# Kernel tuning notes

Hardware: AMD Instinct MI355X
Metric: run time of the kernel (lower is better)

The kernel has to match this reference:

```python
import jax, jax.numpy as jnp
import numpy as np

N = 207      # nodes (hardcoded in source)
D = 128      # hid_dim
H = 8        # attention heads
C = D // H   # head dim
L = 4        # num_layers
B = 16       # batch
NO = 3       # number of orbits
SZ = 69      # orbit size
EPS = 1e-5
SLOPE = 0.2  # GATv2 leaky_relu negative slope


def _cat_matrix():
    # edge category for pair (i,j): off-diag -> pos_i*NO+pos_j, diag -> NO^2+pos_i
    pos = np.arange(N) // SZ
    c = pos[:, None] * NO + pos[None, :]
    np.fill_diagonal(c, NO * NO + pos)
    return c  # [N, N] int


def setup_inputs() -> dict:
    key = jax.random.key(0)
    ks = jax.random.split(key, 16)
    s = 0.05
    rn = lambda k, shape: jax.random.normal(k, shape, jnp.float32) * s
    return {
        "x": jax.random.normal(ks[0], (B, N, 6), jnp.float32),
        "cat": jnp.asarray(_cat_matrix(), jnp.int32),          # [N,N] edge categories
        "emb": rn(ks[1], (NO * NO + NO, D)),                   # edge embedding table
        "in1_W": rn(ks[2], (D, 6)), "in1_b": jnp.zeros((D,)),
        "ln1_g": jnp.ones((D,)), "ln1_b": jnp.zeros((D,)),
        "in2_W": rn(ks[3], (D, D)), "in2_b": jnp.zeros((D,)),
        "ln2_g": jnp.ones((D,)), "ln2_b": jnp.zeros((D,)),
        "Wl": rn(ks[4], (L, D, D)), "bl": jnp.zeros((L, D)),   # GATv2 lin_l (source)
        "Wr": rn(ks[5], (L, D, D)), "br": jnp.zeros((L, D)),   # GATv2 lin_r (target)
        "We": rn(ks[6], (L, D, D)),                            # GATv2 lin_edge (no bias)
        "att": rn(ks[7], (L, H, C)),                           # attention vector
        "cb": jnp.zeros((L, D)),                               # conv output bias
        "pW": rn(ks[8], (L, D, D)), "pb": jnp.zeros((L, D)),   # projection layers
        "lng": jnp.ones((L, D)), "lnb": jnp.zeros((L, D)),     # per-layer LayerNorm
        "oW": rn(ks[9], (2, D)), "ob": jnp.zeros((2,)),        # output layer
    }


def _ln(x, g, b):
    m = x.mean(-1, keepdims=True)
    v = ((x - m) ** 2).mean(-1, keepdims=True)
    return (x - m) * jax.lax.rsqrt(v + EPS) * g + b


def _fwd(cat, x, emb, in1_W, in1_b, ln1_g, ln1_b, in2_W, in2_b, ln2_g, ln2_b,
         Wl, bl, Wr, br, We, att, cb, pW, pb, lng, lnb, oW, ob):
    # input MLP: Linear -> LN -> ReLU -> Linear -> LN
    h = jax.nn.relu(_ln(x @ in1_W.T + in1_b, ln1_g, ln1_b))
    h = _ln(h @ in2_W.T + in2_b, ln2_g, ln2_b)                 # [B,N,D]
    e_all = emb[cat]                                           # [N,N,D] per-edge embedding
    for l in range(L):
        h_prev = h
        gs = (h @ Wl[l].T + bl[l]).reshape(B, N, H, C)         # source transform
        gd = (h @ Wr[l].T + br[l]).reshape(B, N, H, C)         # target transform
        ee = (e_all @ We[l].T).reshape(N, N, H, C)             # edge transform
        # per-edge GATv2 score: edge (i -> j), i source, j target
        z = jax.nn.leaky_relu(gs[:, :, None] + gd[:, None, :] + ee[None], SLOPE)  # [B,i,j,H,C]
        a = jnp.einsum('bijhc,hc->bijh', z, att[l])
        a = jax.nn.softmax(a, axis=1)                          # softmax over sources per target
        o = jnp.einsum('bijh,bihc->bjhc', a, gs).reshape(B, N, D) + cb[l]
        h = h_prev + jax.nn.relu(_ln(o @ pW[l].T + pb[l], lng[l], lnb[l]))
    return h @ oW.T + ob                                       # [B,N,2]


def reference(x, cat, emb, in1_W, in1_b, ln1_g, ln1_b, in2_W, in2_b, ln2_g, ln2_b,
              Wl, bl, Wr, br, We, att, cb, pW, pb, lng, lnb, oW, ob):
    return _fwd(cat, x, emb, in1_W, in1_b, ln1_g, ln1_b, in2_W, in2_b, ln2_g, ln2_b,
                Wl, bl, Wr, br, We, att, cb, pW, pb, lng, lnb, oW, ob)
```

## Files before the change

### kernel.cpp

```cpp
#include <hip/hip_runtime.h>
#include <hip/hip_bf16.h>

#define NN 207
#define DD 128
#define LL 4
#define BB 16
#define ROWS (BB*NN)
#define RB 8
#define LBLK (ROWS/RB)
#define EPSV 1e-5f
#define SLOPE 0.2f
#define GT4B (32*208*4)

template<bool BF>
__device__ __forceinline__ float ldin(const void* p, int i) {
    if (BF) {
        unsigned short u = ((const unsigned short*)p)[i];
        return __uint_as_float(((unsigned)u) << 16);
    } else {
        return ((const float*)p)[i];
    }
}

template<bool BF>
__device__ __forceinline__ void ldw32(const void* W, int base, float* w) {
    if (BF) {
        const uint4* p = (const uint4*)((const unsigned short*)W + base);
#pragma unroll
        for (int q = 0; q < 4; q++) {
            uint4 u = p[q];
            w[q*8+0] = __uint_as_float(u.x << 16);
            w[q*8+1] = __uint_as_float(u.x & 0xFFFF0000u);
            w[q*8+2] = __uint_as_float(u.y << 16);
            w[q*8+3] = __uint_as_float(u.y & 0xFFFF0000u);
            w[q*8+4] = __uint_as_float(u.z << 16);
            w[q*8+5] = __uint_as_float(u.z & 0xFFFF0000u);
            w[q*8+6] = __uint_as_float(u.w << 16);
            w[q*8+7] = __uint_as_float(u.w & 0xFFFF0000u);
        }
    } else {
        const float4* p = (const float4*)((const float*)W + base);
#pragma unroll
        for (int q = 0; q < 8; q++) {
            float4 u = p[q];
            w[q*4+0] = u.x; w[q*4+1] = u.y; w[q*4+2] = u.z; w[q*4+3] = u.w;
        }
    }
}

template<bool BF>
__device__ __forceinline__ float rowdot(const void* W, int rowbase, const float* sh) {
    float acc = 0.f;
    if (BF) {
        const uint4* p = (const uint4*)((const unsigned short*)W + rowbase);
#pragma unroll
        for (int q = 0; q < DD / 8; q++) {
            uint4 u = p[q];
            const float* s = sh + q * 8;
            acc += __uint_as_float(u.x << 16)        * s[0];
            acc += __uint_as_float(u.x & 0xFFFF0000u) * s[1];
            acc += __uint_as_float(u.y << 16)        * s[2];
            acc += __uint_as_float(u.y & 0xFFFF0000u) * s[3];
            acc += __uint_as_float(u.z << 16)        * s[4];
            acc += __uint_as_float(u.z & 0xFFFF0000u) * s[5];
            acc += __uint_as_float(u.w << 16)        * s[6];
            acc += __uint_as_float(u.w & 0xFFFF0000u) * s[7];
        }
    } else {
        const float4* p = (const float4*)((const float*)W + rowbase);
#pragma unroll
        for (int q = 0; q < DD / 4; q++) {
            float4 u = p[q];
            const float* s = sh + q * 4;
            acc += u.x * s[0]; acc += u.y * s[1]; acc += u.z * s[2]; acc += u.w * s[3];
        }
    }
    return acc;
}

__global__ void k_detect(const unsigned int* g1bits, int* flag) {
    *flag = (g1bits[0] == 0x3F803F80u) ? 1 : 0;
}

template<bool BF>
__device__ void et_body(float* sh, const void* emb, const void* We, float* et) {
    int l = blockIdx.x / 12, c = blockIdx.x % 12, d = threadIdx.x;
    sh[d] = ldin<BF>(emb, c * DD + d);
    __syncthreads();
    et[(l * 12 + c) * DD + d] = rowdot<BF>(We, l * DD * DD + d * DD, sh);
}
__global__ void k_et(const int* flag, const void* emb, const void* We, float* et) {
    __shared__ __align__(16) float smem[DD];
    if (*flag) et_body<true>(smem, emb, We, et);
    else       et_body<false>(smem, emb, We, et);
}

template<bool BF>
__device__ void mlp1_body(float* smem, const void* x, const void* W1, const void* b1,
                          const void* g1, const void* bv1, float* tmp) {
    float* s_x   = smem;
    float* so    = s_x + 48;
    float* stats = so + RB * 132;
    int r0 = blockIdx.x * RB, d = threadIdx.x;
    if (d < RB * 6) s_x[d] = ldin<BF>(x, r0 * 6 + d);
    __syncthreads();
    float w6[6];
#pragma unroll
    for (int k = 0; k < 6; k++) w6[k] = ldin<BF>(W1, d * 6 + k);
    float b0 = ldin<BF>(b1, d);
#pragma unroll
    for (int rr = 0; rr < RB; rr++) {
        float a = b0;
#pragma unroll
        for (int k = 0; k < 6; k++) a += w6[k] * s_x[rr * 6 + k];
        so[rr * 132 + d] = a;
    }
    __syncthreads();
    int rr2 = d >> 4, l16 = d & 15;
    float s = 0.f, sq = 0.f;
#pragma unroll
    for (int k = 0; k < 8; k++) { float v = so[rr2 * 132 + l16 + 16 * k]; s += v; sq += v * v; }
    s += __shfl_xor(s, 1); s += __shfl_xor(s, 2); s += __shfl_xor(s, 4); s += __shfl_xor(s, 8);
    sq += __shfl_xor(sq, 1); sq += __shfl_xor(sq, 2); sq += __shfl_xor(sq, 4); sq += __shfl_xor(sq, 8);
    if (l16 == 0) {
        float mean = s * (1.f / DD);
        float var = sq * (1.f / DD) - mean * mean;
        stats[rr2 * 2] = mean; stats[rr2 * 2 + 1] = rsqrtf(var + EPSV);
    }
    __syncthreads();
    float gv = ldin<BF>(g1, d), bb = ldin<BF>(bv1, d);
#pragma unroll
    for (int rr = 0; rr < RB; rr++) {
        float v = (so[rr * 132 + d] - stats[rr * 2]) * stats[rr * 2 + 1] * gv + bb;
        tmp[(r0 + rr) * DD + d] = fmaxf(v, 0.f);
    }
}
__global__ void k_mlp1(const int* flag, const void* x, const void* W1, const void* b1,
                       const void* g1, const void* bv1, float* tmp) {
    __shared__ __align__(16) float smem[48 + RB * 132 + RB * 2];
    if (*flag) mlp1_body<true>(smem, x, W1, b1, g1, bv1, tmp);
    else       mlp1_body<false>(smem, x, W1, b1, g1, bv1, tmp);
}

template<bool BF>
__device__ void lin_body(float* smem, int epi, const float* in, const void* W, int wOff,
                         const void* bias, const void* g, const void* bv, int dOff,
                         float* h) {
    float* sh    = smem;
    float* so    = sh + RB * DD;
    float* stats = so + RB * 132;
    int r0 = blockIdx.x * RB;
    int t = threadIdx.x, d = t & 127, half = t >> 7;
    float4* sh4 = (float4*)sh;
    const float4* iin = (const float4*)(in + r0 * DD);
    sh4[t] = iin[t];
    __syncthreads();
    float acc[4];
    float b0 = ldin<BF>(bias, dOff + d);
#pragma unroll
    for (int rr = 0; rr < 4; rr++) acc[rr] = b0;
#pragma unroll
    for (int c = 0; c < 4; c++) {
        float w[32];
        ldw32<BF>(W, wOff + d * DD + c * 32, w);
#pragma unroll
        for (int rr = 0; rr < 4; rr++) {
            const float* s = sh + (half * 4 + rr) * DD + c * 32;
            float a = acc[rr];
#pragma unroll
            for (int k = 0; k < 32; k++) a += s[k] * w[k];
            acc[rr] = a;
        }
    }
#pragma unroll
    for (int rr = 0; rr < 4; rr++) so[(half * 4 + rr) * 132 + d] = acc[rr];
    __syncthreads();
    int rr2 = t >> 5, l32 = t & 31;
    float s = 0.f, sq = 0.f;
#pragma unroll
    for (int k = 0; k < 4; k++) { float v = so[rr2 * 132 + l32 + 32 * k]; s += v; sq += v * v; }
    s += __shfl_xor(s, 1); s += __shfl_xor(s, 2); s += __shfl_xor(s, 4);
    s += __shfl_xor(s, 8); s += __shfl_xor(s, 16);
    sq += __shfl_xor(sq, 1); sq += __shfl_xor(sq, 2); sq += __shfl_xor(sq, 4);
    sq += __shfl_xor(sq, 8); sq += __shfl_xor(sq, 16);
    if (l32 == 0) {
        float mean = s * (1.f / DD);
        float var = sq * (1.f / DD) - mean * mean;
        stats[rr2 * 2] = mean; stats[rr2 * 2 + 1] = rsqrtf(var + EPSV);
    }
    __syncthreads();
    float gv = ldin<BF>(g, dOff + d), bb = ldin<BF>(bv, dOff + d);
#pragma unroll
    for (int rr = 0; rr < 4; rr++) {
        int row = half * 4 + rr;
        float v = (so[row * 132 + d] - stats[row * 2]) * stats[row * 2 + 1] * gv + bb;
        int rg = r0 + row;
        if (epi) h[(size_t)rg * DD + d] += fmaxf(v, 0.f);
        else     h[(size_t)rg * DD + d] = v;
    }
}
__global__ void k_lin(const int* flag, int epi, const float* in, const void* W, int wOff,
                      const void* bias, const void* g, const void* bv, int dOff, float* h) {
    __shared__ __align__(16) float smem[RB * DD + RB * 132 + RB * 2];
    if (*flag) lin_body<true>(smem, epi, in, W, wOff, bias, g, bv, dOff, h);
    else       lin_body<false>(smem, epi, in, W, wOff, bias, g, bv, dOff, h);
}

template<bool BF>
__device__ void gsgd_body(float* sh, int l, const float* h, const void* Wl, const void* bl,
                          const void* Wr, const void* br, float* gs, float* gd) {
    int r0 = blockIdx.x * RB;
    int t = threadIdx.x, d = t & 127, mat = t >> 7;
    float4* sh4 = (float4*)sh;
    const float4* hin = (const float4*)(h + r0 * DD);
    sh4[t] = hin[t];
    __syncthreads();
    const void* W  = mat ? Wr : Wl;
    const void* bv = mat ? br : bl;
    float acc[RB];
    float b0 = ldin<BF>(bv, l * DD + d);
#pragma unroll
    for (int rr = 0; rr < RB; rr++) acc[rr] = b0;
#pragma unroll
    for (int c = 0; c < 4; c++) {
        float w[32];
        ldw32<BF>(W, l * DD * DD + d * DD + c * 32, w);
#pragma unroll
        for (int rr = 0; rr < RB; rr++) {
            const float* s = sh + rr * DD + c * 32;
            float a = acc[rr];
#pragma unroll
            for (int k = 0; k < 32; k++) a += s[k] * w[k];
            acc[rr] = a;
        }
    }
    float* outp = mat ? gd : gs;
#pragma unroll
    for (int rr = 0; rr < RB; rr++) outp[(size_t)(r0 + rr) * DD + d] = acc[rr];
}
__global__ void k_gsgd(const int* flag, int l, const float* h, const void* Wl, const void* bl,
                       const void* Wr, const void* br, float* gs, float* gd) {
    __shared__ __align__(16) float smem[RB * DD];
    if (*flag) gsgd_body<true>(smem, l, h, Wl, bl, Wr, br, gs, gd);
    else       gsgd_body<false>(smem, l, h, Wl, bl, Wr, br, gs, gd);
}

__global__ void __launch_bounds__(256, 4) k_trans(const float* gs, float* gs_t4) {
    __shared__ __align__(16) float sb[RB * 132];
    int q = blockIdx.x;
    int batch = q / 26, pr = q - batch * 26;
    int brow0 = pr * 8;
    int nrows = NN - brow0; if (nrows > RB) nrows = RB;
    int t = threadIdx.x;
    int srow = t >> 5, se = t & 31;
    int cr = srow < nrows ? srow : nrows - 1;
    ((float4*)(sb + srow * 132))[se] =
        ((const float4*)(gs + (size_t)(batch * NN + brow0 + cr) * DD))[se];
    __syncthreads();
    int d4 = t >> 3, ii = t & 7;
    if (ii < nrows) {
        float4 v;
        v.x = sb[ii * 132 + d4 * 4 + 0];
        v.y = sb[ii * 132 + d4 * 4 + 1];
        v.z = sb[ii * 132 + d4 * 4 + 2];
        v.w = sb[ii * 132 + d4 * 4 + 3];
        ((float4*)(gs_t4 + (size_t)batch * GT4B))[d4 * 208 + brow0 + ii] = v;
    }
}

#define ATTN_SMEM (12*132 + 128 + 8*212 + 8 + 128 + 207)
template<bool BF>
__device__ void attn_body(float* smem, int l, const float* gs, const float* gd, const float* et,
                          const float* gs_t4, const int* cat, const void* att, const void* cb,
                          float* o) {
    float* s_ge   = smem;
    float* s_att  = s_ge + 12 * 132;
    float* s_pe   = s_att + 128;
    float* s_inv  = s_pe + 8 * 212;
    float* s_part = s_inv + 8;
    int*   s_cat  = (int*)(s_part + 128);
    int p = blockIdx.x;
    int r = (p & 7) * (ROWS / 8) + (p >> 3);
    int t = threadIdx.x, d = t & 127, seg = t >> 7;
    int b = r / NN, j = r - b * NN;
    if (t < DD) s_att[t] = ldin<BF>(att, l * DD + t);
    for (int idx = t; idx < NN; idx += 256) s_cat[idx] = cat[idx * NN + j];
    for (int idx = t; idx < 12 * DD; idx += 256) {
        int c = idx >> 7, k = idx & 127;
        s_ge[c * 132 + k] = et[l * 12 * DD + idx] + gd[(size_t)r * DD + k];
    }
    __syncthreads();
    const float* gsb = gs + (size_t)b * NN * DD;
    if (t < NN) {
        const float4* gt = ((const float4*)(gs_t4 + (size_t)b * GT4B)) + t;
        const float4* ge = (const float4*)(s_ge + s_cat[t] * 132);
        const float4* at = (const float4*)s_att;
        float acc[8];
#pragma unroll
        for (int hh = 0; hh < 8; hh++) acc[hh] = 0.f;
#pragma unroll
        for (int q = 0; q < 32; q++) {
            float4 g4 = gt[q * 208];
            float4 e4 = ge[q], a4 = at[q];
            float z0 = g4.x + e4.x, z1 = g4.y + e4.y, z2 = g4.z + e4.z, z3 = g4.w + e4.w;
            z0 = fmaxf(z0, SLOPE * z0); z1 = fmaxf(z1, SLOPE * z1);
            z2 = fmaxf(z2, SLOPE * z2); z3 = fmaxf(z3, SLOPE * z3);
            acc[q >> 2] += a4.x * z0 + a4.y * z1 + a4.z * z2 + a4.w * z3;
        }
#pragma unroll
        for (int hh = 0; hh < 8; hh++) s_pe[hh * 212 + t] = acc[hh];
    }
    __syncthreads();
    if (t < 128) {
        int hh = t >> 4, l16 = t & 15;
        float vals[13]; float mx = -1e30f;
#pragma unroll
        for (int k = 0; k < 13; k++) {
            int i = l16 + 16 * k;
            vals[k] = (i < NN) ? s_pe[hh * 212 + i] : -1e30f;
            mx = fmaxf(mx, vals[k]);
        }
        mx = fmaxf(mx, __shfl_xor(mx, 1)); mx = fmaxf(mx, __shfl_xor(mx, 2));
        mx = fmaxf(mx, __shfl_xor(mx, 4)); mx = fmaxf(mx, __shfl_xor(mx, 8));
        float sum = 0.f;
#pragma unroll
        for (int k = 0; k < 13; k++) {
            int i = l16 + 16 * k;
            float e = (i < NN) ? __expf(vals[k] - mx) : 0.f;
            if (i < 208) s_pe[hh * 212 + i] = e;
            sum += e;
        }
        sum += __shfl_xor(sum, 1); sum += __shfl_xor(sum, 2);
        sum += __shfl_xor(sum, 4); sum += __shfl_xor(sum, 8);
        if (l16 == 0) s_inv[hh] = 1.f / sum;
    }
    __syncthreads();
    {
        int hh = d >> 4;
        const float* ep = s_pe + hh * 212;
        const float* gp = gsb + d;
        float a0 = 0.f, a1 = 0.f, a2 = 0.f, a3 = 0.f;
        int i = seg * 104;
        int iend = seg ? NN : 104;
        for (; i + 8 <= iend; i += 8) {
            float g0 = gp[(i+0)*DD], g1 = gp[(i+1)*DD], g2 = gp[(i+2)*DD], g3 = gp[(i+3)*DD];
            float g4 = gp[(i+4)*DD], g5 = gp[(i+5)*DD], g6 = gp[(i+6)*DD], g7 = gp[(i+7)*DD];
            a0 = fmaf(ep[i+0], g0, a0); a1 = fmaf(ep[i+1], g1, a1);
            a2 = fmaf(ep[i+2], g2, a2); a3 = fmaf(ep[i+3], g3, a3);
            a0 = fmaf(ep[i+4], g4, a0); a1 = fmaf(ep[i+5], g5, a1);
            a2 = fmaf(ep[i+6], g6, a2); a3 = fmaf(ep[i+7], g7, a3);
        }
        for (; i < iend; i++) a0 = fmaf(ep[i], gp[i * DD], a0);
        float part = a0 + a1 + a2 + a3;
        if (seg) s_part[d] = part;
        __syncthreads();
        if (!seg) o[(size_t)r * DD + d] = (part + s_part[d]) * s_inv[hh] + ldin<BF>(cb, l * DD + d);
    }
}
__global__ void __launch_bounds__(256, 4)
k_attn(const int* flag, int l, const float* gs, const float* gd, const float* et,
       const float* gs_t4, const int* cat, const void* att, const void* cb,
       float* o) {
    __shared__ __align__(16) float smem[ATTN_SMEM];
    if (*flag) attn_body<true>(smem, l, gs, gd, et, gs_t4, cat, att, cb, o);
    else       attn_body<false>(smem, l, gs, gd, et, gs_t4, cat, att, cb, o);
}

__device__ __forceinline__ void blk_red2(float& a, float& b, float* red) {
#pragma unroll
    for (int m = 32; m; m >>= 1) { a += __shfl_xor(a, m); b += __shfl_xor(b, m); }
    int wid = threadIdx.x >> 6;
    if ((threadIdx.x & 63) == 0) { red[wid * 2] = a; red[wid * 2 + 1] = b; }
    __syncthreads();
    a = red[0] + red[2];
    b = red[1] + red[3];
    __syncthreads();
}
template<bool BF>
__device__ void out_body(float* red, const float* h, const void* oW, const void* ob, void* out) {
    int r = blockIdx.x, d = threadIdx.x;
    float hv = h[(size_t)r * DD + d];
    float p0 = hv * ldin<BF>(oW, d);
    float p1 = hv * ldin<BF>(oW, DD + d);
    blk_red2(p0, p1, red);
    if (d < 2) {
        float v = (d == 0 ? p0 : p1) + ldin<BF>(ob, d);
        if (BF) ((__hip_bfloat16*)out)[r * 2 + d] = __float2bfloat16(v);
        else    ((float*)out)[r * 2 + d] = v;
    }
}
__global__ void k_out(const int* flag, const float* h, const void* oW, const void* ob, void* out) {
    __shared__ float red[4];
    if (*flag) out_body<true>(red, h, oW, ob, out);
    else       out_body<false>(red, h, oW, ob, out);
}

extern "C" void kernel_launch(void* const* d_in, const int* in_sizes, int n_in,
                              void* d_out, int out_size, void* d_ws, size_t ws_size,
                              hipStream_t stream) {
    const void* x     = d_in[0];
    const int*  cat   = (const int*)d_in[1];
    const void* emb   = d_in[2];
    const void* in1W  = d_in[3];
    const void* in1b  = d_in[4];
    const void* ln1g  = d_in[5];
    const void* ln1b  = d_in[6];
    const void* in2W  = d_in[7];
    const void* in2b  = d_in[8];
    const void* ln2g  = d_in[9];
    const void* ln2b  = d_in[10];
    const void* Wl    = d_in[11];
    const void* bl    = d_in[12];
    const void* Wr    = d_in[13];
    const void* br    = d_in[14];
    const void* We    = d_in[15];
    const void* att   = d_in[16];
    const void* cb    = d_in[17];
    const void* pW    = d_in[18];
    const void* pb    = d_in[19];
    const void* lng   = d_in[20];
    const void* lnb   = d_in[21];
    const void* oW    = d_in[22];
    const void* ob    = d_in[23];

    float* ws  = (float*)d_ws;
    int*  flag = (int*)d_ws;
    float* h     = ws + 16;
    float* gs    = h    + ROWS * DD;
    float* gd    = gs   + ROWS * DD;
    float* o     = gd   + ROWS * DD;
    float* et    = o    + ROWS * DD;
    float* gs_t4 = et   + LL * 12 * DD;
    float* tmp   = gs;

    k_detect<<<1, 1, 0, stream>>>((const unsigned int*)ln1g, flag);
    k_et<<<LL * 12, DD, 0, stream>>>(flag, emb, We, et);
    k_mlp1<<<LBLK, DD, 0, stream>>>(flag, x, in1W, in1b, ln1g, ln1b, tmp);
    k_lin<<<LBLK, 256, 0, stream>>>(flag, 0, tmp, in2W, 0, in2b, ln2g, ln2b, 0, h);
    for (int l = 0; l < LL; l++) {
        k_gsgd<<<LBLK, 256, 0, stream>>>(flag, l, h, Wl, bl, Wr, br, gs, gd);
        k_trans<<<BB * 26, 256, 0, stream>>>(gs, gs_t4);
        k_attn<<<ROWS, 256, 0, stream>>>(flag, l, gs, gd, et, gs_t4, cat, att, cb, o);
        k_lin<<<LBLK, 256, 0, stream>>>(flag, 1, o, pW, l * DD * DD, pb, lng, lnb, l * DD, h);
    }
    k_out<<<ROWS, DD, 0, stream>>>(flag, h, oW, ob, d_out);
}
```

Baseline: 368.5 us.

## Process two target nodes per attention block to reuse source features

Each attention block now handles two target nodes (j and j+104) of the same batch, so the transposed source features loaded for scoring and the gs rows read in the aggregation step are shared across both targets. The grid shrinks from ROWS blocks to BB*104 blocks. The aggregation is reorganised so all 256 threads do float4 loads over 8 source segments, followed by a shared-memory reduction. In exchange it uses more shared memory and registers per block and has fewer blocks, which may lower occupancy.

```diff
diff --git a/kernel.cpp b/kernel.cpp
--- a/kernel.cpp
+++ b/kernel.cpp
@@ -268,93 +268,131 @@
     }
 }
 
-#define ATTN_SMEM (12*132 + 128 + 8*212 + 8 + 128 + 207)
+#define ATTN_SMEM (1584*2 + 128 + 1696*2 + 16 + 1024 + 416)
 template<bool BF>
 __device__ void attn_body(float* smem, int l, const float* gs, const float* gd, const float* et,
                           const float* gs_t4, const int* cat, const void* att, const void* cb,
                           float* o) {
-    float* s_ge   = smem;
-    float* s_att  = s_ge + 12 * 132;
-    float* s_pe   = s_att + 128;
-    float* s_inv  = s_pe + 8 * 212;
-    float* s_part = s_inv + 8;
-    int*   s_cat  = (int*)(s_part + 128);
+    float* s_ge1 = smem;
+    float* s_ge2 = s_ge1 + 1584;
+    float* s_att = s_ge2 + 1584;
+    float* s_pe1 = s_att + 128;
+    float* s_pe2 = s_pe1 + 1696;
+    float* s_inv = s_pe2 + 1696;
+    float* s_prt = s_inv + 16;
+    int*   s_cat1 = (int*)(s_prt + 1024);
+    int*   s_cat2 = s_cat1 + 208;
     int p = blockIdx.x;
-    int r = (p & 7) * (ROWS / 8) + (p >> 3);
-    int t = threadIdx.x, d = t & 127, seg = t >> 7;
-    int b = r / NN, j = r - b * NN;
+    int kk = (p & 7) * 208 + (p >> 3);
+    int b = kk / 104, k = kk - b * 104;
+    int j1 = k, j2 = k + 104;
+    bool has2 = (k < 103);
+    int r1 = b * NN + j1, r2 = b * NN + j2;
+    int t = threadIdx.x;
     if (t < DD) s_att[t] = ldin<BF>(att, l * DD + t);
-    for (int idx = t; idx < NN; idx += 256) s_cat[idx] = cat[idx * NN + j];
+    for (int idx = t; idx < NN; idx += 256) {
+        s_cat1[idx] = cat[idx * NN + j1];
+        s_cat2[idx] = has2 ? cat[idx * NN + j2] : 0;
+    }
     for (int idx = t; idx < 12 * DD; idx += 256) {
-        int c = idx >> 7, k = idx & 127;
-        s_ge[c * 132 + k] = et[l * 12 * DD + idx] + gd[(size_t)r * DD + k];
-    }
-    __syncthreads();
-    const float* gsb = gs + (size_t)b * NN * DD;
+        int c = idx >> 7, kd = idx & 127;
+        float ev = et[l * 12 * DD + idx];
+        s_ge1[c * 132 + kd] = ev + gd[(size_t)r1 * DD + kd];
+        s_ge2[c * 132 + kd] = has2 ? (ev + gd[(size_t)r2 * DD + kd]) : 0.f;
+    }
+    __syncthreads();
     if (t < NN) {
-        const float4* gt = ((const float4*)(gs_t4 + (size_t)b * GT4B)) + t;
-        const float4* ge = (const float4*)(s_ge + s_cat[t] * 132);
-        const float4* at = (const float4*)s_att;
-        float acc[8];
-#pragma unroll
-        for (int hh = 0; hh < 8; hh++) acc[hh] = 0.f;
+        const float4* gt  = ((const float4*)(gs_t4 + (size_t)b * GT4B)) + t;
+        const float4* ge1 = (const float4*)(s_ge1 + s_cat1[t] * 132);
+        const float4* ge2 = (const float4*)(s_ge2 + s_cat2[t] * 132);
+        const float4* at  = (const float4*)s_att;
+        float a1[8], a2[8];
+#pragma unroll
+        for (int hh = 0; hh < 8; hh++) { a1[hh] = 0.f; a2[hh] = 0.f; }
 #pragma unroll
         for (int q = 0; q < 32; q++) {
             float4 g4 = gt[q * 208];
-            float4 e4 = ge[q], a4 = at[q];
-            float z0 = g4.x + e4.x, z1 = g4.y + e4.y, z2 = g4.z + e4.z, z3 = g4.w + e4.w;
+            float4 A  = at[q];
+            float4 e1 = ge1[q];
+            float z0 = g4.x + e1.x, z1 = g4.y + e1.y, z2 = g4.z + e1.z, z3 = g4.w + e1.w;
             z0 = fmaxf(z0, SLOPE * z0); z1 = fmaxf(z1, SLOPE * z1);
             z2 = fmaxf(z2, SLOPE * z2); z3 = fmaxf(z3, SLOPE * z3);
-            acc[q >> 2] += a4.x * z0 + a4.y * z1 + a4.z * z2 + a4.w * z3;
-        }
-#pragma unroll
-        for (int hh = 0; hh < 8; hh++) s_pe[hh * 212 + t] = acc[hh];
-    }
-    __syncthreads();
-    if (t < 128) {
-        int hh = t >> 4, l16 = t & 15;
+            a1[q >> 2] += A.x * z0 + A.y * z1 + A.z * z2 + A.w * z3;
+            float4 e2 = ge2[q];
+            float y0 = g4.x + e2.x, y1 = g4.y + e2.y, y2 = g4.z + e2.z, y3 = g4.w + e2.w;
+            y0 = fmaxf(y0, SLOPE * y0); y1 = fmaxf(y1, SLOPE * y1);
+            y2 = fmaxf(y2, SLOPE * y2); y3 = fmaxf(y3, SLOPE * y3);
+            a2[q >> 2] += A.x * y0 + A.y * y1 + A.z * y2 + A.w * y3;
+        }
+#pragma unroll
+        for (int hh = 0; hh < 8; hh++) {
+            s_pe1[hh * 212 + t] = a1[hh];
+            s_pe2[hh * 212 + t] = a2[hh];
+        }
+    }
+    __syncthreads();
+    {
+        int g = t >> 4, l16 = t & 15;
+        float* pe = (g < 8) ? s_pe1 : s_pe2;
+        int hh = g & 7;
         float vals[13]; float mx = -1e30f;
 #pragma unroll
-        for (int k = 0; k < 13; k++) {
-            int i = l16 + 16 * k;
-            vals[k] = (i < NN) ? s_pe[hh * 212 + i] : -1e30f;
-            mx = fmaxf(mx, vals[k]);
+        for (int kq = 0; kq < 13; kq++) {
+            int i = l16 + 16 * kq;
+            vals[kq] = (i < NN) ? pe[hh * 212 + i] : -1e30f;
+            mx = fmaxf(mx, vals[kq]);
         }
         mx = fmaxf(mx, __shfl_xor(mx, 1)); mx = fmaxf(mx, __shfl_xor(mx, 2));
         mx = fmaxf(mx, __shfl_xor(mx, 4)); mx = fmaxf(mx, __shfl_xor(mx, 8));
         float sum = 0.f;
 #pragma unroll
-        for (int k = 0; k < 13; k++) {
-            int i = l16 + 16 * k;
-            float e = (i < NN) ? __expf(vals[k] - mx) : 0.f;
-            if (i < 208) s_pe[hh * 212 + i] = e;
+        for (int kq = 0; kq < 13; kq++) {
+            int i = l16 + 16 * kq;
+            float e = (i < NN) ? __expf(vals[kq] - mx) : 0.f;
+            if (i < 208) pe[hh * 212 + i] = e;
             sum += e;
         }
         sum += __shfl_xor(sum, 1); sum += __shfl_xor(sum, 2);
         sum += __shfl_xor(sum, 4); sum += __shfl_xor(sum, 8);
-        if (l16 == 0) s_inv[hh] = 1.f / sum;
-    }
-    __syncthreads();
+        if (l16 == 0) s_inv[g] = 1.f / sum;
+    }
+    __syncthreads();
+    float4 p1, p2;
+    int d4 = t & 31, sg = t >> 5;
     {
-        int hh = d >> 4;
-        const float* ep = s_pe + hh * 212;
-        const float* gp = gsb + d;
-        float a0 = 0.f, a1 = 0.f, a2 = 0.f, a3 = 0.f;
-        int i = seg * 104;
-        int iend = seg ? NN : 104;
-        for (; i + 8 <= iend; i += 8) {
-            float g0 = gp[(i+0)*DD], g1 = gp[(i+1)*DD], g2 = gp[(i+2)*DD], g3 = gp[(i+3)*DD];
-            float g4 = gp[(i+4)*DD], g5 = gp[(i+5)*DD], g6 = gp[(i+6)*DD], g7 = gp[(i+7)*DD];
-            a0 = fmaf(ep[i+0], g0, a0); a1 = fmaf(ep[i+1], g1, a1);
-            a2 = fmaf(ep[i+2], g2, a2); a3 = fmaf(ep[i+3], g3, a3);
-            a0 = fmaf(ep[i+4], g4, a0); a1 = fmaf(ep[i+5], g5, a1);
-            a2 = fmaf(ep[i+6], g6, a2); a3 = fmaf(ep[i+7], g7, a3);
-        }
-        for (; i < iend; i++) a0 = fmaf(ep[i], gp[i * DD], a0);
-        float part = a0 + a1 + a2 + a3;
-        if (seg) s_part[d] = part;
-        __syncthreads();
-        if (!seg) o[(size_t)r * DD + d] = (part + s_part[d]) * s_inv[hh] + ldin<BF>(cb, l * DD + d);
+        int hh = d4 >> 2;
+        const float4* g4p = ((const float4*)(gs + (size_t)b * NN * DD)) + d4;
+        const float* e1 = s_pe1 + hh * 212;
+        const float* e2 = s_pe2 + hh * 212;
+        int i0 = sg * 26;
+        int i1 = i0 + 26; if (i1 > NN) i1 = NN;
+        p1.x = p1.y = p1.z = p1.w = 0.f;
+        p2.x = p2.y = p2.z = p2.w = 0.f;
+        for (int i = i0; i < i1; i++) {
+            float4 g4 = g4p[i * 32];
+            float w1 = e1[i], w2 = e2[i];
+            p1.x = fmaf(w1, g4.x, p1.x); p1.y = fmaf(w1, g4.y, p1.y);
+            p1.z = fmaf(w1, g4.z, p1.z); p1.w = fmaf(w1, g4.w, p1.w);
+            p2.x = fmaf(w2, g4.x, p2.x); p2.y = fmaf(w2, g4.y, p2.y);
+            p2.z = fmaf(w2, g4.z, p2.z); p2.w = fmaf(w2, g4.w, p2.w);
+        }
+    }
+    ((float4*)s_prt)[sg * 32 + d4] = p1;
+    __syncthreads();
+    if (t < 128) {
+        float sum = 0.f;
+#pragma unroll
+        for (int s = 0; s < 8; s++) sum += s_prt[s * 128 + t];
+        o[(size_t)r1 * DD + t] = sum * s_inv[t >> 4] + ldin<BF>(cb, l * DD + t);
+    }
+    __syncthreads();
+    ((float4*)s_prt)[sg * 32 + d4] = p2;
+    __syncthreads();
+    if (t < 128 && has2) {
+        float sum = 0.f;
+#pragma unroll
+        for (int s = 0; s < 8; s++) sum += s_prt[s * 128 + t];
+        o[(size_t)r2 * DD + t] = sum * s_inv[8 + (t >> 4)] + ldin<BF>(cb, l * DD + t);
     }
 }
 __global__ void __launch_bounds__(256, 4)
@@ -440,7 +478,7 @@
     for (int l = 0; l < LL; l++) {
         k_gsgd<<<LBLK, 256, 0, stream>>>(flag, l, h, Wl, bl, Wr, br, gs, gd);
         k_trans<<<BB * 26, 256, 0, stream>>>(gs, gs_t4);
-        k_attn<<<ROWS, 256, 0, stream>>>(flag, l, gs, gd, et, gs_t4, cat, att, cb, o);
+        k_attn<<<BB * 104, 256, 0, stream>>>(flag, l, gs, gd, et, gs_t4, cat, att, cb, o);
         k_lin<<<LBLK, 256, 0, stream>>>(flag, 1, o, pW, l * DD * DD, pb, lng, lnb, l * DD, h);
     }
     k_out<<<ROWS, DD, 0, stream>>>(flag, h, oW, ob, d_out);
```

After: 366.2 us. No clear change (-0.6%).
